# Performance work log

Measured on AMD Instinct MI355X. Metric: run time of the kernel, lower is better.

## Reference

```python
import jax, jax.numpy as jnp
import numpy as np

SHARED_DIM = 512
ENC_IN = 512
LATENT = 16
BATCH = 65536
NUM_CLASSES = 16


def setup_inputs() -> dict:
    key = jax.random.key(0)
    ks = jax.random.split(key, 12)
    s = 1.0 / np.sqrt(SHARED_DIM)
    si = 1.0 / np.sqrt(ENC_IN)
    return {
        "x": jax.random.normal(ks[0], (BATCH, ENC_IN), dtype=jnp.float32),
        # shared MLP: two ReLU hiddens + identity output (rlkit Mlp)
        "W0": jax.random.uniform(ks[1], (SHARED_DIM, ENC_IN), jnp.float32, -si, si),
        "b0": jnp.zeros((SHARED_DIM,), jnp.float32),
        "W1": jax.random.uniform(ks[2], (SHARED_DIM, SHARED_DIM), jnp.float32, -s, s),
        "b1": jnp.zeros((SHARED_DIM,), jnp.float32),
        "W2": jax.random.uniform(ks[3], (SHARED_DIM, SHARED_DIM), jnp.float32, -s, s),
        "b2": jnp.zeros((SHARED_DIM,), jnp.float32),
        # class encoder (router)
        "Wc": jax.random.uniform(ks[4], (NUM_CLASSES, SHARED_DIM), jnp.float32, -s, s),
        "bc": jnp.zeros((NUM_CLASSES,), jnp.float32),
        # per-class gaussian experts, stacked: [K, 2*latent, shared_dim]
        "Wg": jax.random.uniform(ks[5], (NUM_CLASSES, 2 * LATENT, SHARED_DIM), jnp.float32, -s, s),
        "bg": jnp.zeros((NUM_CLASSES, 2 * LATENT), jnp.float32),
    }


def reference(x, W0, b0, W1, b1, W2, b2, Wc, bc, Wg, bg):
    # shared encoder: ReLU MLP with identity output layer
    m = jax.nn.relu(x @ W0.T + b0)
    m = jax.nn.relu(m @ W1.T + b1)
    m = m @ W2.T + b2                      # [B, D]
    # router: softmax over classes, then most-likely class per sample
    y_probs = jax.nn.softmax(m @ Wc.T + bc, axis=-1)   # [B, K]
    y = jnp.argmax(y_probs, axis=1)                    # [B]
    # evaluate ALL per-class experts densely (as the original does)
    mu_sigma = jnp.einsum('bd,ked->bke', m, Wg) + bg   # [B, K, 2L]
    mu = mu_sigma[..., :LATENT]                        # Normal mean; sampler='mean'
    # gather the selected class's mean per sample
    z = jnp.take_along_axis(mu, y[:, None, None], axis=1)[:, 0, :]  # [B, L]
    return (z, y)
```

## Files before the change

### kernel.cpp

```cpp
#include <hip/hip_runtime.h>
#include <hip/hip_bf16.h>

typedef __attribute__((ext_vector_type(8))) short short8;
typedef __attribute__((ext_vector_type(16))) float floatx16;
typedef __attribute__((ext_vector_type(4))) float floatx4;

constexpr int MM = 65536;
constexpr int KK = 512;
constexpr int NN = 512;

#define GM 128
#define GN 128
#define GK 32
#define LDT 40

__device__ __forceinline__ unsigned short bf16_rn(float v) {
  unsigned u = __float_as_uint(v);
  return (unsigned short)((u + 0x7FFFu + ((u >> 16) & 1u)) >> 16);
}
__device__ __forceinline__ float bf16_to_f32(unsigned short h) {
  return __uint_as_float((unsigned)h << 16);
}

__global__ __launch_bounds__(256) void split_kernel(
    const float* __restrict__ src, unsigned short* __restrict__ h,
    unsigned short* __restrict__ l, int n4) {
  int i = blockIdx.x * 256 + threadIdx.x;
  if (i >= n4) return;
  float4 v = ((const float4*)src)[i];
  ushort4 hv, lv;
  hv.x = bf16_rn(v.x); lv.x = bf16_rn(v.x - bf16_to_f32(hv.x));
  hv.y = bf16_rn(v.y); lv.y = bf16_rn(v.y - bf16_to_f32(hv.y));
  hv.z = bf16_rn(v.z); lv.z = bf16_rn(v.z - bf16_to_f32(hv.z));
  hv.w = bf16_rn(v.w); lv.w = bf16_rn(v.w - bf16_to_f32(hv.w));
  ((ushort4*)h)[i] = hv;
  ((ushort4*)l)[i] = lv;
}

template<bool RELU, bool SPLIT>
__global__ __launch_bounds__(256, 2) void gemm_mfma(
    const unsigned short* __restrict__ Ah, const unsigned short* __restrict__ Al,
    const unsigned short* __restrict__ Wh, const unsigned short* __restrict__ Wl,
    const float* __restrict__ bias,
    unsigned short* __restrict__ Ch, unsigned short* __restrict__ Cl,
    float* __restrict__ Cf) {
  __shared__ unsigned short sAh[GM][LDT], sAl[GM][LDT];
  __shared__ unsigned short sBh[GN][LDT], sBl[GN][LDT];
  const int tid = threadIdx.x;
  const int lane = tid & 63;
  const int wid = tid >> 6;
  const int wr = wid >> 1;
  const int wc = wid & 1;
  const int bm = blockIdx.x, bn = blockIdx.y;
  const size_t Abase = (size_t)bm * GM * KK;
  const size_t Bbase = (size_t)bn * GN * KK;

  floatx16 acc[2][2];
#pragma unroll
  for (int i = 0; i < 2; ++i)
#pragma unroll
    for (int j = 0; j < 2; ++j)
#pragma unroll
      for (int r = 0; r < 16; ++r) acc[i][j][r] = 0.f;

  for (int k0 = 0; k0 < KK; k0 += GK) {
#pragma unroll
    for (int t = 0; t < 2; ++t) {
      int s = tid + t * 256;
      int row = s >> 2;
      int cc = (s & 3) * 8;
      size_t goff = (size_t)row * KK + k0 + cc;
      *(short8*)&sAh[row][cc] = *(const short8*)(Ah + Abase + goff);
      *(short8*)&sAl[row][cc] = *(const short8*)(Al + Abase + goff);
      *(short8*)&sBh[row][cc] = *(const short8*)(Wh + Bbase + goff);
      *(short8*)&sBl[row][cc] = *(const short8*)(Wl + Bbase + goff);
    }
    __syncthreads();

#pragma unroll
    for (int ks = 0; ks < 2; ++ks) {
      const int ko = ks * 16 + (lane >> 5) * 8;
      short8 fah[2], fal[2], fbh[2], fbl[2];
#pragma unroll
      for (int ri = 0; ri < 2; ++ri) {
        int row = wr * 64 + ri * 32 + (lane & 31);
        fah[ri] = *(const short8*)&sAh[row][ko];
        fal[ri] = *(const short8*)&sAl[row][ko];
      }
#pragma unroll
      for (int si = 0; si < 2; ++si) {
        int col = wc * 64 + si * 32 + (lane & 31);
        fbh[si] = *(const short8*)&sBh[col][ko];
        fbl[si] = *(const short8*)&sBl[col][ko];
      }
#pragma unroll
      for (int ri = 0; ri < 2; ++ri)
#pragma unroll
        for (int si = 0; si < 2; ++si) {
          acc[ri][si] = __builtin_amdgcn_mfma_f32_32x32x16_bf16(fah[ri], fbh[si], acc[ri][si], 0, 0, 0);
          acc[ri][si] = __builtin_amdgcn_mfma_f32_32x32x16_bf16(fah[ri], fbl[si], acc[ri][si], 0, 0, 0);
          acc[ri][si] = __builtin_amdgcn_mfma_f32_32x32x16_bf16(fal[ri], fbh[si], acc[ri][si], 0, 0, 0);
        }
    }
    __syncthreads();
  }

#pragma unroll
  for (int si = 0; si < 2; ++si) {
    int col = bn * GN + wc * 64 + si * 32 + (lane & 31);
    float bv = bias[col];
#pragma unroll
    for (int ri = 0; ri < 2; ++ri) {
#pragma unroll
      for (int r = 0; r < 16; ++r) {
        int row = bm * GM + wr * 64 + ri * 32 + (r & 3) + 8 * (r >> 2) + 4 * (lane >> 5);
        float v = acc[ri][si][r] + bv;
        if (RELU) v = fmaxf(v, 0.f);
        size_t idx = (size_t)row * NN + col;
        if (SPLIT) {
          unsigned short h = bf16_rn(v);
          Ch[idx] = h;
          Cl[idx] = bf16_rn(v - bf16_to_f32(h));
        } else {
          Cf[idx] = v;
        }
      }
    }
  }
}

__global__ __launch_bounds__(256, 2) void gemm_mu(
    const unsigned short* __restrict__ Ahm, const unsigned short* __restrict__ Wh,
    const float* __restrict__ bias, float* __restrict__ Cf) {
  __shared__ unsigned short sAh[GM][LDT];
  __shared__ unsigned short sBh[GN][LDT];
  const int tid = threadIdx.x;
  const int lane = tid & 63;
  const int wid = tid >> 6;
  const int wr = wid >> 1;
  const int wc = wid & 1;
  const int bm = blockIdx.x, bn = blockIdx.y;
  const size_t Abase = (size_t)bm * GM * KK;
  const size_t Bbase = (size_t)bn * GN * KK;

  floatx16 acc[2][2];
#pragma unroll
  for (int i = 0; i < 2; ++i)
#pragma unroll
    for (int j = 0; j < 2; ++j)
#pragma unroll
      for (int r = 0; r < 16; ++r) acc[i][j][r] = 0.f;

  for (int k0 = 0; k0 < KK; k0 += GK) {
#pragma unroll
    for (int t = 0; t < 2; ++t) {
      int s = tid + t * 256;
      int row = s >> 2;
      int cc = (s & 3) * 8;
      size_t goff = (size_t)row * KK + k0 + cc;
      *(short8*)&sAh[row][cc] = *(const short8*)(Ahm + Abase + goff);
      *(short8*)&sBh[row][cc] = *(const short8*)(Wh + Bbase + goff);
    }
    __syncthreads();
#pragma unroll
    for (int ks = 0; ks < 2; ++ks) {
      const int ko = ks * 16 + (lane >> 5) * 8;
      short8 fa[2], fb[2];
#pragma unroll
      for (int ri = 0; ri < 2; ++ri)
        fa[ri] = *(const short8*)&sAh[wr * 64 + ri * 32 + (lane & 31)][ko];
#pragma unroll
      for (int si = 0; si < 2; ++si)
        fb[si] = *(const short8*)&sBh[wc * 64 + si * 32 + (lane & 31)][ko];
#pragma unroll
      for (int ri = 0; ri < 2; ++ri)
#pragma unroll
        for (int si = 0; si < 2; ++si)
          acc[ri][si] = __builtin_amdgcn_mfma_f32_32x32x16_bf16(fa[ri], fb[si], acc[ri][si], 0, 0, 0);
    }
    __syncthreads();
  }

#pragma unroll
  for (int si = 0; si < 2; ++si) {
    int col = bn * GN + wc * 64 + si * 32 + (lane & 31);
    float bv = bias[col];
#pragma unroll
    for (int ri = 0; ri < 2; ++ri)
#pragma unroll
      for (int r = 0; r < 16; ++r) {
        int row = bm * GM + wr * 64 + ri * 32 + (r & 3) + 8 * (r >> 2) + 4 * (lane >> 5);
        Cf[(size_t)row * 256 + col] = acc[ri][si][r] + bv;
      }
  }
}

__global__ __launch_bounds__(256) void logits_kernel(
    const unsigned short* __restrict__ mh, const unsigned short* __restrict__ ml,
    const unsigned short* __restrict__ wch, const unsigned short* __restrict__ wcl,
    const float* __restrict__ bc, float* __restrict__ y_out) {
  __shared__ unsigned short smh[64][LDT], sml[64][LDT];
  __shared__ float slog[64][17];
  const int tid = threadIdx.x;
  const int lane = tid & 63;
  const int wid = tid >> 6;
  const size_t row0 = (size_t)blockIdx.x * 64;
  const int fr = lane & 15;
  const int fq = lane >> 4;

  floatx4 acc = {0.f, 0.f, 0.f, 0.f};
  const unsigned short* bh = wch + fr * 512 + fq * 8;
  const unsigned short* bl = wcl + fr * 512 + fq * 8;

  for (int k0 = 0; k0 < 512; k0 += 32) {
    {
      int row = tid >> 2, cc = (tid & 3) * 8;
      size_t g = (row0 + row) * 512 + k0 + cc;
      *(short8*)&smh[row][cc] = *(const short8*)(mh + g);
      *(short8*)&sml[row][cc] = *(const short8*)(ml + g);
    }
    __syncthreads();
    short8 ah = *(const short8*)&smh[wid * 16 + fr][fq * 8];
    short8 al = *(const short8*)&sml[wid * 16 + fr][fq * 8];
    short8 fbh = *(const short8*)(bh + k0);
    short8 fbl = *(const short8*)(bl + k0);
    acc = __builtin_amdgcn_mfma_f32_16x16x32_bf16(ah, fbh, acc, 0, 0, 0);
    acc = __builtin_amdgcn_mfma_f32_16x16x32_bf16(ah, fbl, acc, 0, 0, 0);
    acc = __builtin_amdgcn_mfma_f32_16x16x32_bf16(al, fbh, acc, 0, 0, 0);
    __syncthreads();
  }
#pragma unroll
  for (int r = 0; r < 4; ++r)
    slog[wid * 16 + fq * 4 + r][fr] = acc[r] + bc[fr];
  __syncthreads();
  if (tid < 64) {
    float best = slog[tid][0];
    int bi = 0;
#pragma unroll
    for (int j = 1; j < 16; ++j) {
      float v = slog[tid][j];
      if (v > best) { best = v; bi = j; }
    }
    y_out[row0 + tid] = (float)bi;
  }
}

__global__ __launch_bounds__(256) void prep_wg(
    const float* __restrict__ Wg, const float* __restrict__ bg,
    unsigned short* __restrict__ wgh, float* __restrict__ wgb) {
  int gid = blockIdx.x * 256 + threadIdx.x;
  if (gid >= 32768) return;
  int r = gid >> 7;
  int c4 = (gid & 127) * 4;
  int k = r >> 4, e = r & 15;
  float4 v = *(const float4*)(Wg + ((size_t)k * 32 + e) * 512 + c4);
  ushort4 h;
  h.x = bf16_rn(v.x); h.y = bf16_rn(v.y); h.z = bf16_rn(v.z); h.w = bf16_rn(v.w);
  *(ushort4*)(wgh + (size_t)r * 512 + c4) = h;
  if (c4 == 0) wgb[r] = bg[k * 32 + e];
}

__global__ __launch_bounds__(256) void select_kernel(
    const float* __restrict__ mu, const float* __restrict__ y_in,
    float* __restrict__ z_out) {
  int gid = blockIdx.x * 256 + threadIdx.x;
  int b = gid >> 4, e = gid & 15;
  int y = (int)y_in[b];
  z_out[gid] = mu[(size_t)b * 256 + y * 16 + e];
}

extern "C" void kernel_launch(void* const* d_in, const int* in_sizes, int n_in,
                              void* d_out, int out_size, void* d_ws, size_t ws_size,
                              hipStream_t stream) {
  const float* x  = (const float*)d_in[0];
  const float* W0 = (const float*)d_in[1];
  const float* b0 = (const float*)d_in[2];
  const float* W1 = (const float*)d_in[3];
  const float* b1 = (const float*)d_in[4];
  const float* W2 = (const float*)d_in[5];
  const float* b2 = (const float*)d_in[6];
  const float* Wc = (const float*)d_in[7];
  const float* bc = (const float*)d_in[8];
  const float* Wg = (const float*)d_in[9];
  const float* bg = (const float*)d_in[10];

  const size_t NEL = (size_t)MM * KK;
  unsigned short* Ah = (unsigned short*)d_ws;
  unsigned short* Al = Ah + NEL;
  unsigned short* Bh = Al + NEL;
  unsigned short* Bl = Bh + NEL;
  float* mu_all = (float*)Ah;
  unsigned short* wch = Al;
  unsigned short* wcl = Al + 8192;
  unsigned short* wgh = Al + 16384;
  float* wgb = (float*)(Al + 16384 + 131072);

  unsigned short* w0h = (unsigned short*)d_out;
  unsigned short* w0l = w0h + 262144;
  unsigned short* w1h = w0l + 262144;
  unsigned short* w1l = w1h + 262144;
  unsigned short* w2h = w1l + 262144;
  unsigned short* w2l = w2h + 262144;

  float* z_out = (float*)d_out;
  float* y_out = z_out + (size_t)MM * 16;

  split_kernel<<<(int)(NEL / 4 / 256), 256, 0, stream>>>(x, Ah, Al, (int)(NEL / 4));
  split_kernel<<<256, 256, 0, stream>>>(W0, w0h, w0l, 65536);
  split_kernel<<<256, 256, 0, stream>>>(W1, w1h, w1l, 65536);
  split_kernel<<<256, 256, 0, stream>>>(W2, w2h, w2l, 65536);

  dim3 grid(MM / GM, NN / GN);
  gemm_mfma<true , true ><<<grid, 256, 0, stream>>>(Ah, Al, w0h, w0l, b0, Bh, Bl, nullptr);
  gemm_mfma<true , true ><<<grid, 256, 0, stream>>>(Bh, Bl, w1h, w1l, b1, Ah, Al, nullptr);
  gemm_mfma<false, true ><<<grid, 256, 0, stream>>>(Ah, Al, w2h, w2l, b2, Bh, Bl, nullptr);

  split_kernel<<<8, 256, 0, stream>>>(Wc, wch, wcl, 2048);
  prep_wg<<<128, 256, 0, stream>>>(Wg, bg, wgh, wgb);

  logits_kernel<<<MM / 64, 256, 0, stream>>>(Bh, Bl, wch, wcl, bc, y_out);
  gemm_mu<<<dim3(MM / GM, 2), 256, 0, stream>>>(Bh, wgh, wgb, mu_all);
  select_kernel<<<MM * 16 / 256, 256, 0, stream>>>(mu_all, y_out, z_out);
}
```

Baseline: 686.0 us.

## Load GEMM tiles directly into LDS with global_load_lds and XOR swizzle

Replaces the register-staged global-to-shared tile copies in both GEMM kernels with direct global-to-LDS loads. Each wavefront now owns one operand tile. The padded shared-memory layout is replaced by an unpadded layout with an XOR swizzle on 16-byte chunks to avoid bank conflicts on the MFMA fragment reads. This cuts VGPR traffic and load instructions, but relies on the swizzle mapping being correct and on the builtin's per-lane LDS addressing semantics.

New measurement: 707.1 us. +3.1%, slower.

```diff
diff --git a/kernel.cpp b/kernel.cpp
--- a/kernel.cpp
+++ b/kernel.cpp
@@ -4,6 +4,9 @@
 typedef __attribute__((ext_vector_type(8))) short short8;
 typedef __attribute__((ext_vector_type(16))) float floatx16;
 typedef __attribute__((ext_vector_type(4))) float floatx4;
+
+#define AS1 __attribute__((address_space(1)))
+#define AS3 __attribute__((address_space(3)))
 
 constexpr int MM = 65536;
 constexpr int KK = 512;
@@ -44,8 +47,8 @@
     const float* __restrict__ bias,
     unsigned short* __restrict__ Ch, unsigned short* __restrict__ Cl,
     float* __restrict__ Cf) {
-  __shared__ unsigned short sAh[GM][LDT], sAl[GM][LDT];
-  __shared__ unsigned short sBh[GN][LDT], sBl[GN][LDT];
+  __shared__ __align__(16) unsigned short sAh[GM][GK], sAl[GM][GK];
+  __shared__ __align__(16) unsigned short sBh[GN][GK], sBl[GN][GK];
   const int tid = threadIdx.x;
   const int lane = tid & 63;
   const int wid = tid >> 6;
@@ -55,6 +58,15 @@
   const size_t Abase = (size_t)bm * GM * KK;
   const size_t Bbase = (size_t)bn * GN * KK;
 
+  const unsigned short* gsrc; unsigned short* ldst; size_t tb;
+  if (wid == 0)      { gsrc = Ah; tb = Abase; ldst = &sAh[0][0]; }
+  else if (wid == 1) { gsrc = Al; tb = Abase; ldst = &sAl[0][0]; }
+  else if (wid == 2) { gsrc = Wh; tb = Bbase; ldst = &sBh[0][0]; }
+  else               { gsrc = Wl; tb = Bbase; ldst = &sBl[0][0]; }
+  const int rowl = lane >> 2;
+  const int gch  = (lane & 3) ^ (rowl & 3);
+  const size_t laneoff = (size_t)rowl * KK + gch * 8;
+
   floatx16 acc[2][2];
 #pragma unroll
   for (int i = 0; i < 2; ++i)
@@ -65,33 +77,30 @@
 
   for (int k0 = 0; k0 < KK; k0 += GK) {
 #pragma unroll
-    for (int t = 0; t < 2; ++t) {
-      int s = tid + t * 256;
-      int row = s >> 2;
-      int cc = (s & 3) * 8;
-      size_t goff = (size_t)row * KK + k0 + cc;
-      *(short8*)&sAh[row][cc] = *(const short8*)(Ah + Abase + goff);
-      *(short8*)&sAl[row][cc] = *(const short8*)(Al + Abase + goff);
-      *(short8*)&sBh[row][cc] = *(const short8*)(Wh + Bbase + goff);
-      *(short8*)&sBl[row][cc] = *(const short8*)(Wl + Bbase + goff);
+    for (int j = 0; j < 8; ++j) {
+      const unsigned short* g = gsrc + tb + (size_t)(j * 16) * KK + k0 + laneoff;
+      __builtin_amdgcn_global_load_lds((const AS1 unsigned int*)g,
+                                       (AS3 unsigned int*)(ldst + j * 16 * GK),
+                                       16, 0, 0);
     }
     __syncthreads();
 
 #pragma unroll
     for (int ks = 0; ks < 2; ++ks) {
-      const int ko = ks * 16 + (lane >> 5) * 8;
+      const int ch = ks * 2 + (lane >> 5);
+      const int sw = (ch ^ (lane & 3)) * 8;
       short8 fah[2], fal[2], fbh[2], fbl[2];
 #pragma unroll
       for (int ri = 0; ri < 2; ++ri) {
         int row = wr * 64 + ri * 32 + (lane & 31);
-        fah[ri] = *(const short8*)&sAh[row][ko];
-        fal[ri] = *(const short8*)&sAl[row][ko];
+        fah[ri] = *(const short8*)((const unsigned short*)sAh + row * GK + sw);
+        fal[ri] = *(const short8*)((const unsigned short*)sAl + row * GK + sw);
       }
 #pragma unroll
       for (int si = 0; si < 2; ++si) {
         int col = wc * 64 + si * 32 + (lane & 31);
-        fbh[si] = *(const short8*)&sBh[col][ko];
-        fbl[si] = *(const short8*)&sBl[col][ko];
+        fbh[si] = *(const short8*)((const unsigned short*)sBh + col * GK + sw);
+        fbl[si] = *(const short8*)((const unsigned short*)sBl + col * GK + sw);
       }
 #pragma unroll
       for (int ri = 0; ri < 2; ++ri)
@@ -132,8 +141,8 @@
 __global__ __launch_bounds__(256, 2) void gemm_mu(
     const unsigned short* __restrict__ Ahm, const unsigned short* __restrict__ Wh,
     const float* __restrict__ bias, float* __restrict__ Cf) {
-  __shared__ unsigned short sAh[GM][LDT];
-  __shared__ unsigned short sBh[GN][LDT];
+  __shared__ __align__(16) unsigned short sAh[GM][GK];
+  __shared__ __align__(16) unsigned short sBh[GN][GK];
   const int tid = threadIdx.x;
   const int lane = tid & 63;
   const int wid = tid >> 6;
@@ -143,6 +152,14 @@
   const size_t Abase = (size_t)bm * GM * KK;
   const size_t Bbase = (size_t)bn * GN * KK;
 
+  const unsigned short* gsrc = (wid < 2) ? Ahm : Wh;
+  const size_t tb = (wid < 2) ? Abase : Bbase;
+  unsigned short* ldst = (wid < 2) ? &sAh[0][0] : &sBh[0][0];
+  const int rbase = (wid & 1) * 64;
+  const int rowl = lane >> 2;
+  const int gch  = (lane & 3) ^ (rowl & 3);
+  const size_t laneoff = (size_t)rowl * KK + gch * 8;
+
   floatx16 acc[2][2];
 #pragma unroll
   for (int i = 0; i < 2; ++i)
@@ -153,25 +170,29 @@
 
   for (int k0 = 0; k0 < KK; k0 += GK) {
 #pragma unroll
-    for (int t = 0; t < 2; ++t) {
-      int s = tid + t * 256;
-      int row = s >> 2;
-      int cc = (s & 3) * 8;
-      size_t goff = (size_t)row * KK + k0 + cc;
-      *(short8*)&sAh[row][cc] = *(const short8*)(Ahm + Abase + goff);
-      *(short8*)&sBh[row][cc] = *(const short8*)(Wh + Bbase + goff);
+    for (int j = 0; j < 4; ++j) {
+      const int r0 = rbase + j * 16;
+      const unsigned short* g = gsrc + tb + (size_t)r0 * KK + k0 + laneoff;
+      __builtin_amdgcn_global_load_lds((const AS1 unsigned int*)g,
+                                       (AS3 unsigned int*)(ldst + r0 * GK),
+                                       16, 0, 0);
     }
     __syncthreads();
 #pragma unroll
     for (int ks = 0; ks < 2; ++ks) {
-      const int ko = ks * 16 + (lane >> 5) * 8;
+      const int ch = ks * 2 + (lane >> 5);
+      const int sw = (ch ^ (lane & 3)) * 8;
       short8 fa[2], fb[2];
 #pragma unroll
-      for (int ri = 0; ri < 2; ++ri)
-        fa[ri] = *(const short8*)&sAh[wr * 64 + ri * 32 + (lane & 31)][ko];
-#pragma unroll
-      for (int si = 0; si < 2; ++si)
-        fb[si] = *(const short8*)&sBh[wc * 64 + si * 32 + (lane & 31)][ko];
+      for (int ri = 0; ri < 2; ++ri) {
+        int row = wr * 64 + ri * 32 + (lane & 31);
+        fa[ri] = *(const short8*)((const unsigned short*)sAh + row * GK + sw);
+      }
+#pragma unroll
+      for (int si = 0; si < 2; ++si) {
+        int col = wc * 64 + si * 32 + (lane & 31);
+        fb[si] = *(const short8*)((const unsigned short*)sBh + col * GK + sw);
+      }
 #pragma unroll
       for (int ri = 0; ri < 2; ++ri)
 #pragma unroll
```
